# Optimization experiments

Hardware: AMD Instinct MI355X
Metric: run time of the kernel (lower is better)

Reference implementation:

```python
import jax, jax.numpy as jnp
import numpy as np

B, C, H, W = 64, 1280, 16, 16
S = H * W  # 256 spatial positions


def setup_inputs() -> dict:
    key = jax.random.key(0)
    kx, kk, kq, kv, kr, ka = jax.random.split(key, 6)
    x = jax.random.normal(kx, (B, C, H, W), dtype=jnp.float32)
    scale = 0.02
    Wk = jax.random.normal(kk, (C, C), dtype=jnp.float32) * scale
    Wq = jax.random.normal(kq, (C, C), dtype=jnp.float32) * scale
    Wv = jax.random.normal(kv, (C, C), dtype=jnp.float32) * scale
    Wr = jax.random.normal(kr, (C, C), dtype=jnp.float32) * scale
    # nn.Parameter(torch.zeros(1)) in the original; init nonzero so the
    # attention branch actually contributes.
    alpha = jax.random.normal(ka, (1,), dtype=jnp.float32) * 0.1
    return {"x": x, "Wk": Wk, "Wq": Wq, "Wv": Wv, "Wr": Wr, "alpha": alpha}


def reference(x, Wk, Wq, Wv, Wr, alpha):
    b, c = x.shape[0], x.shape[1]
    s = x.shape[2] * x.shape[3]
    xf = x.reshape(b, c, s)  # [B, C, S]
    # 1x1 convs == per-position channel matmuls
    K = jnp.einsum("oc,bcs->bos", Wk, xf)  # [B, C, S]
    Q = jnp.einsum("oc,bcs->bos", Wq, xf)
    V = jnp.einsum("oc,bcs->bos", Wv, xf)
    # scores[b,i,j] = sum_c K[b,c,i] * Q[b,c,j]
    scores = jnp.einsum("bci,bcj->bij", K, Q) / (c ** 0.5)  # [B, S, S]
    # torch.nn.Softmax2d on a 3D tensor applies softmax over dim=-3,
    # i.e. across the BATCH axis here (faithful to the original code).
    A = jax.nn.softmax(scores, axis=0)
    # attended[b,c,i] = sum_j A[b,i,j] * V[b,c,j]
    att = jnp.einsum("bij,bcj->bci", A, V)  # [B, C, S]
    refined = jnp.einsum("oc,bcs->bos", Wr, att).reshape(x.shape)
    out = alpha * refined + x  # use_alpha=True, skip connection
    return out
```

## Files before the change

kernel.cpp:

```cpp
#include <hip/hip_runtime.h>
#include <hip/hip_bf16.h>
#include <cstdint>
#include <cmath>

#define B_ 64
#define C_ 1280
#define S_ 256

typedef __attribute__((ext_vector_type(8))) short short8;
typedef __attribute__((ext_vector_type(4))) float f32x4;

typedef const __attribute__((address_space(1))) char gch;
typedef __attribute__((address_space(3))) char lch;

__device__ __forceinline__ void gload_lds16(const void* g, void* l) {
    __builtin_amdgcn_global_load_lds((gch*)g, (lch*)l, 16, 0, 0);
}

__device__ __forceinline__ unsigned short f2bu(float f) {
    __hip_bfloat16 h = __float2bfloat16(f);
    return *reinterpret_cast<unsigned short*>(&h);
}

__global__ void prep_weights(const float* __restrict__ Wk, const float* __restrict__ Wq,
                             const float* __restrict__ Wv, const float* __restrict__ Wr,
                             __hip_bfloat16* __restrict__ WqT, __hip_bfloat16* __restrict__ WkT,
                             __hip_bfloat16* __restrict__ WvT, __hip_bfloat16* __restrict__ Wrb) {
    __shared__ float tile[32][33];
    int z = blockIdx.z;
    const float* src = (z == 0) ? Wq : (z == 1) ? Wk : (z == 2) ? Wv : Wr;
    __hip_bfloat16* dst = (z == 0) ? WqT : (z == 1) ? WkT : (z == 2) ? WvT : Wrb;
    int r0 = blockIdx.x * 32, c0 = blockIdx.y * 32;
    int tx = threadIdx.x, ty = threadIdx.y;
    if (z == 3) {
#pragma unroll
        for (int dy = 0; dy < 32; dy += 8) {
            int idx = (r0 + ty + dy) * C_ + c0 + tx;
            dst[idx] = __float2bfloat16(src[idx]);
        }
        return;
    }
#pragma unroll
    for (int dy = 0; dy < 32; dy += 8)
        tile[ty + dy][tx] = src[(long)(r0 + ty + dy) * C_ + c0 + tx];
    __syncthreads();
#pragma unroll
    for (int dy = 0; dy < 32; dy += 8)
        dst[(long)(c0 + ty + dy) * C_ + r0 + tx] = __float2bfloat16(tile[tx][ty + dy]);
}

__global__ void transpose_cvt(const float* __restrict__ x, __hip_bfloat16* __restrict__ xT) {
    __shared__ float tile[32][33];
    int b = blockIdx.z;
    int s0 = blockIdx.x * 32, c0 = blockIdx.y * 32;
    int tx = threadIdx.x, ty = threadIdx.y;
    const float* xb = x + (long)b * C_ * S_;
#pragma unroll
    for (int dy = 0; dy < 32; dy += 8)
        tile[ty + dy][tx] = xb[(long)(c0 + ty + dy) * S_ + s0 + tx];
    __syncthreads();
    __hip_bfloat16* xTb = xT + (long)b * S_ * C_;
#pragma unroll
    for (int dy = 0; dy < 32; dy += 8)
        xTb[(long)(s0 + ty + dy) * C_ + c0 + tx] = __float2bfloat16(tile[tx][ty + dy]);
}

__global__ void softmax_b(const float* __restrict__ scores, __hip_bfloat16* __restrict__ Abf) {
    int tid = blockIdx.x * blockDim.x + threadIdx.x;
    float r[64];
    float mx = -1e30f;
#pragma unroll
    for (int b = 0; b < 64; ++b) {
        r[b] = scores[(long)b * 65536 + tid];
        mx = fmaxf(mx, r[b]);
    }
    float sum = 0.f;
#pragma unroll
    for (int b = 0; b < 64; ++b) {
        r[b] = __expf(r[b] - mx);
        sum += r[b];
    }
    float inv = 1.0f / sum;
#pragma unroll
    for (int b = 0; b < 64; ++b)
        Abf[(long)b * 65536 + tid] = __float2bfloat16(r[b] * inv);
}


#define PH_TOP()                                                \
    do {                                                        \
        __builtin_amdgcn_sched_barrier(0);                      \
        __builtin_amdgcn_s_barrier();                           \
        asm volatile("s_waitcnt lgkmcnt(0)" ::: "memory");      \
        __builtin_amdgcn_sched_barrier(0);                      \
        __builtin_amdgcn_s_setprio(1);                          \
    } while (0)

#define PH_BOT()                                                \
    do {                                                        \
        __builtin_amdgcn_s_setprio(0);                          \
        __builtin_amdgcn_sched_barrier(0);                      \
        __builtin_amdgcn_s_barrier();                           \
    } while (0)

#define PH_BOT_WAIT(LAST_)                                          \
    do {                                                            \
        __builtin_amdgcn_s_setprio(0);                              \
        __builtin_amdgcn_sched_barrier(0);                          \
        if (LAST_) asm volatile("s_waitcnt vmcnt(0)" ::: "memory"); \
        else       asm volatile("s_waitcnt vmcnt(2)" ::: "memory"); \
        __builtin_amdgcn_s_barrier();                               \
    } while (0)

#define MFMA_Q(MO, NO, BFV)                                                                        \
    _Pragma("unroll") for (int m = 0; m < 4; ++m) {                                                \
        _Pragma("unroll") for (int n = 0; n < 2; ++n) {                                            \
            acc[m + MO][n + NO] = __builtin_amdgcn_mfma_f32_16x16x32_bf16(                         \
                af[m][0], BFV[n][0], acc[m + MO][n + NO], 0, 0, 0);                                \
            acc[m + MO][n + NO] = __builtin_amdgcn_mfma_f32_16x16x32_bf16(                         \
                af[m][1], BFV[n][1], acc[m + MO][n + NO], 0, 0, 0);                                \
        }                                                                                          \
    }

#define LOAD_A(SLOT, RO)                                  \
    _Pragma("unroll") for (int m = 0; m < 4; ++m) {       \
        af[m][0] = RD(SLOT, (RO) + m * 16 + l15, 0);      \
        af[m][1] = RD(SLOT, (RO) + m * 16 + l15, 1);      \
    }

#define LOAD_B(SLOT, BFV, NO)                                    \
    _Pragma("unroll") for (int n = 0; n < 2; ++n) {              \
        BFV[n][0] = RD(SLOT, rB0 + ((NO) + n) * 16 + l15, 0);    \
        BFV[n][1] = RD(SLOT, rB0 + ((NO) + n) * 16 + l15, 1);    \
    }

__global__ __launch_bounds__(512, 2) void gemm8p(
    const __hip_bfloat16* __restrict__ A, const __hip_bfloat16* __restrict__ Bm,
    __hip_bfloat16* __restrict__ Cc, int lda, int ldb, int ldc,
    int Kd, int tilesN, int nwg, int vTile,
    __hip_bfloat16* __restrict__ Vb) {
    __shared__ char lds[131072];

    int bid = blockIdx.x;
    int cpx = nwg >> 3;
    int swz = (bid & 7) * cpx + (bid >> 3);
    int tm = swz / tilesN, tn = swz - tm * tilesN;

    int t = threadIdx.x;
    int lane = t & 63, w = t >> 6;
    int wm = w >> 2, wn = w & 3;
    int l15 = lane & 15, lhi = lane >> 4;
    int rB0 = (wn & 1) * 64;
    const int sA0 = wm, sB0 = 2 + (wn >> 1);
    const int sA1 = 4 + wm, sB1 = 6 + (wn >> 1);

    const __hip_bfloat16* aT = A + (long)tm * 256 * lda;
    const __hip_bfloat16* bT = Bm + (long)tn * 256 * ldb;

    int srow = t >> 3;
    int sc = ((t & 7) ^ (srow & 7)) * 8;
    const __hip_bfloat16* stA = aT + (long)srow * lda + sc;
    const __hip_bfloat16* stB = bT + (long)srow * ldb + sc;

    auto STAGE = [&](int kt, int j) {
        const __hip_bfloat16* p;
        long ldg;
        if (j < 2) { p = stA + (long)j * 128 * lda + kt * 64; ldg = lda; }
        else       { p = stB + (long)(j - 2) * 128 * ldb + kt * 64; ldg = ldb; }
        char* slot = lds + (((kt & 1) * 4 + j) << 14);
        gload_lds16(p, slot + t * 16);
        gload_lds16(p + 64 * ldg, slot + t * 16 + 8192);
    };

    auto RD = [&](int slotIdx, int row, int kk) -> short8 {
        const char* p = lds + (slotIdx << 14) + row * 128 +
                        ((((kk << 2) + lhi) ^ (row & 7)) << 4);
        return *reinterpret_cast<const short8*>(p);
    };

    f32x4 acc[8][4];
#pragma unroll
    for (int i = 0; i < 8; ++i)
#pragma unroll
        for (int j = 0; j < 4; ++j) acc[i][j] = (f32x4){0.f, 0.f, 0.f, 0.f};

    short8 af[4][2], b0v[2][2], b1v[2][2];

    STAGE(0, 0); STAGE(0, 1); STAGE(0, 2); STAGE(0, 3); STAGE(1, 0);
    asm volatile("s_waitcnt vmcnt(2)" ::: "memory");
    __builtin_amdgcn_s_barrier();
    __builtin_amdgcn_sched_barrier(0);

    const int NTH = Kd >> 7;
    for (int i = 0; i < NTH; ++i) {
        const bool last = (i == NTH - 1);
        const int kt0 = 2 * i, kt1 = 2 * i + 1;

        LOAD_A(sA0, 0)
        LOAD_B(sB0, b0v, 0)
        STAGE(kt1, 1);
        PH_TOP();
        MFMA_Q(0, 0, b0v)
        PH_BOT();

        LOAD_B(sB0, b1v, 2)
        STAGE(kt1, 2);
        PH_TOP();
        MFMA_Q(0, 2, b1v)
        PH_BOT();

        LOAD_A(sA0, 64)
        STAGE(kt1, 3);
        PH_TOP();
        MFMA_Q(4, 2, b1v)
        PH_BOT();

        if (!last) STAGE(kt0 + 2, 0);
        PH_TOP();
        MFMA_Q(4, 0, b0v)
        PH_BOT_WAIT(last);

        LOAD_A(sA1, 0)
        LOAD_B(sB1, b0v, 0)
        if (!last) STAGE(kt0 + 2, 1);
        PH_TOP();
        MFMA_Q(0, 0, b0v)
        PH_BOT();

        LOAD_B(sB1, b1v, 2)
        if (!last) STAGE(kt0 + 2, 2);
        PH_TOP();
        MFMA_Q(0, 2, b1v)
        PH_BOT();

        LOAD_A(sA1, 64)
        if (!last) STAGE(kt0 + 2, 3);
        PH_TOP();
        MFMA_Q(4, 2, b1v)
        PH_BOT();

        if (!last) STAGE(kt0 + 3, 0);
        PH_TOP();
        MFMA_Q(4, 0, b0v)
        __builtin_amdgcn_s_setprio(0);
        __builtin_amdgcn_sched_barrier(0);
        if (!last) asm volatile("s_waitcnt vmcnt(2)" ::: "memory");
        __builtin_amdgcn_s_barrier();
    }

    if (tn < vTile) {
        long crow0 = (long)tm * 256 + wm * 128;
        int cc0 = tn * 256 + wn * 64;
#pragma unroll
        for (int m = 0; m < 8; ++m) {
            long gm = crow0 + m * 16 + lhi * 4;
#pragma unroll
            for (int n = 0; n < 4; ++n) {
                int gn = cc0 + n * 16 + l15;
#pragma unroll
                for (int r = 0; r < 4; ++r)
                    Cc[(gm + r) * ldc + gn] = __float2bfloat16(acc[m][n][r]);
            }
        }
    } else {
        unsigned short* Vus = (unsigned short*)Vb;
        int cb0 = (tn - vTile) * 256 + wn * 64;
#pragma unroll
        for (int m = 0; m < 8; ++m) {
            int s0 = wm * 128 + m * 16 + lhi * 4;
#pragma unroll
            for (int n = 0; n < 4; ++n) {
                int c = cb0 + n * 16 + l15;
                ushort4 pk;
                pk.x = f2bu(acc[m][n][0]);
                pk.y = f2bu(acc[m][n][1]);
                pk.z = f2bu(acc[m][n][2]);
                pk.w = f2bu(acc[m][n][3]);
                *reinterpret_cast<ushort4*>(&Vus[((long)(tm * 1280 + c) << 8) + s0]) = pk;
            }
        }
    }
}

template <int MODE>
__global__ __launch_bounds__(256) void gemm_tn(
    const __hip_bfloat16* __restrict__ A, long aBatch, int lda,
    const __hip_bfloat16* __restrict__ Bm, long bBatch, int ldb,
    void* __restrict__ Cp, long cBatch, int ldc,
    int Kd, int tilesM, int tilesN, float scale) {
    __shared__ __hip_bfloat16 lA[128 * 32];
    __shared__ __hip_bfloat16 lB[128 * 32];

    int tiles = tilesM * tilesN;
    int blk = blockIdx.x;
    int b = blk / tiles;
    int rem = blk - b * tiles;
    int tm = rem / tilesN;
    int tn = rem - tm * tilesN;

    int t = threadIdx.x;
    int lane = t & 63;
    int w = t >> 6;
    int wm = w >> 1, wn = w & 1;
    int lane15 = lane & 15, lhi = lane >> 4;

    const __hip_bfloat16* Ab = A + (long)b * aBatch + (long)tm * 128 * lda;
    const __hip_bfloat16* Bb = Bm + (long)b * bBatch + (long)tn * 128 * ldb;

    f32x4 acc[4][4];
#pragma unroll
    for (int i = 0; i < 4; ++i)
#pragma unroll
        for (int j = 0; j < 4; ++j) acc[i][j] = (f32x4){0.f, 0.f, 0.f, 0.f};

    int e0 = t * 8;
    int r0 = e0 >> 5;
    int c0e = e0 & 31;

    for (int k0 = 0; k0 < Kd; k0 += 32) {
        gload_lds16(Ab + (long)r0 * lda + k0 + c0e, lA + e0);
        gload_lds16(Ab + (long)(r0 + 64) * lda + k0 + c0e, lA + 2048 + e0);
        gload_lds16(Bb + (long)r0 * ldb + k0 + c0e, lB + e0);
        gload_lds16(Bb + (long)(r0 + 64) * ldb + k0 + c0e, lB + 2048 + e0);
        __syncthreads();

        short8 af[4], bf[4];
#pragma unroll
        for (int i = 0; i < 4; ++i)
            af[i] = *reinterpret_cast<const short8*>(lA + (wm * 64 + i * 16 + lane15) * 32 + lhi * 8);
#pragma unroll
        for (int j = 0; j < 4; ++j)
            bf[j] = *reinterpret_cast<const short8*>(lB + (wn * 64 + j * 16 + lane15) * 32 + lhi * 8);
#pragma unroll
        for (int i = 0; i < 4; ++i)
#pragma unroll
            for (int j = 0; j < 4; ++j)
                acc[i][j] = __builtin_amdgcn_mfma_f32_16x16x32_bf16(af[i], bf[j], acc[i][j], 0, 0, 0);
        __syncthreads();
    }

    long cOff = (long)b * cBatch;
    float* Cb = (float*)Cp + cOff;
#pragma unroll
    for (int i = 0; i < 4; ++i) {
        int gm = tm * 128 + wm * 64 + i * 16 + lhi * 4;
#pragma unroll
        for (int j = 0; j < 4; ++j) {
            int gn = tn * 128 + wn * 64 + j * 16 + lane15;
#pragma unroll
            for (int r = 0; r < 4; ++r)
                Cb[(long)(gm + r) * ldc + gn] = acc[i][j][r] * scale;
        }
    }
}

__global__ __launch_bounds__(256) void gemm_weights(
    const __hip_bfloat16* __restrict__ WqT, const __hip_bfloat16* __restrict__ WkT,
    const __hip_bfloat16* __restrict__ Wrb, const __hip_bfloat16* __restrict__ WvT,
    __hip_bfloat16* __restrict__ Bcat, float scale) {
    __shared__ __hip_bfloat16 lA[128 * 32];
    __shared__ __hip_bfloat16 lB[128 * 32];

    int blk = blockIdx.x;
    const __hip_bfloat16 *A, *Bm;
    __hip_bfloat16* Cb;
    float sc;
    int rem;
    if (blk < 100) { A = WqT; Bm = WkT; Cb = Bcat; sc = scale; rem = blk; }
    else { A = Wrb; Bm = WvT; Cb = Bcat + 1280 * 1280; sc = 1.f; rem = blk - 100; }
    int tm = rem / 10, tn = rem - tm * 10;

    int t = threadIdx.x;
    int lane = t & 63;
    int w = t >> 6;
    int wm = w >> 1, wn = w & 1;
    int lane15 = lane & 15, lhi = lane >> 4;

    const __hip_bfloat16* Ab = A + (long)tm * 128 * C_;
    const __hip_bfloat16* Bb = Bm + (long)tn * 128 * C_;

    f32x4 acc[4][4];
#pragma unroll
    for (int i = 0; i < 4; ++i)
#pragma unroll
        for (int j = 0; j < 4; ++j) acc[i][j] = (f32x4){0.f, 0.f, 0.f, 0.f};

    int e0 = t * 8;
    int r0 = e0 >> 5;
    int c0e = e0 & 31;

    for (int k0 = 0; k0 < C_; k0 += 32) {
        gload_lds16(Ab + (long)r0 * C_ + k0 + c0e, lA + e0);
        gload_lds16(Ab + (long)(r0 + 64) * C_ + k0 + c0e, lA + 2048 + e0);
        gload_lds16(Bb + (long)r0 * C_ + k0 + c0e, lB + e0);
        gload_lds16(Bb + (long)(r0 + 64) * C_ + k0 + c0e, lB + 2048 + e0);
        __syncthreads();

        short8 af[4], bf[4];
#pragma unroll
        for (int i = 0; i < 4; ++i)
            af[i] = *reinterpret_cast<const short8*>(lA + (wm * 64 + i * 16 + lane15) * 32 + lhi * 8);
#pragma unroll
        for (int j = 0; j < 4; ++j)
            bf[j] = *reinterpret_cast<const short8*>(lB + (wn * 64 + j * 16 + lane15) * 32 + lhi * 8);
#pragma unroll
        for (int i = 0; i < 4; ++i)
#pragma unroll
            for (int j = 0; j < 4; ++j)
                acc[i][j] = __builtin_amdgcn_mfma_f32_16x16x32_bf16(af[i], bf[j], acc[i][j], 0, 0, 0);
        __syncthreads();
    }

#pragma unroll
    for (int i = 0; i < 4; ++i) {
        int gm = tm * 128 + wm * 64 + i * 16 + lhi * 4;
#pragma unroll
        for (int j = 0; j < 4; ++j) {
            int gn = tn * 128 + wn * 64 + j * 16 + lane15;
#pragma unroll
            for (int r = 0; r < 4; ++r)
                Cb[(long)(gm + r) * C_ + gn] = __float2bfloat16(acc[i][j][r] * sc);
        }
    }
}

__global__ __launch_bounds__(256) void final_att(
    const __hip_bfloat16* __restrict__ Abf, const __hip_bfloat16* __restrict__ P,
    const float* __restrict__ x, const float* __restrict__ alphaPtr,
    float* __restrict__ out) {
    __shared__ __hip_bfloat16 lA[128 * 32];
    __shared__ __hip_bfloat16 lB[128 * 32];

    int blk = blockIdx.x;
    int b = blk / 20;
    int rem = blk - b * 20;
    int tm = rem / 10, tn = rem - tm * 10;

    int t = threadIdx.x;
    int lane = t & 63;
    int w = t >> 6;
    int wm = w >> 1, wn = w & 1;
    int lane15 = lane & 15, lhi = lane >> 4;

    const __hip_bfloat16* Ab = Abf + (long)b * (S_ * S_) + (long)tm * 128 * S_;
    const __hip_bfloat16* Bb = P + (long)b * (C_ * S_) + (long)tn * 128 * S_;

    f32x4 acc[4][4];
#pragma unroll
    for (int i = 0; i < 4; ++i)
#pragma unroll
        for (int j = 0; j < 4; ++j) acc[i][j] = (f32x4){0.f, 0.f, 0.f, 0.f};

    int e0 = t * 8;
    int r0 = e0 >> 5;
    int c0e = e0 & 31;

#pragma unroll
    for (int k0 = 0; k0 < S_; k0 += 32) {
        gload_lds16(Ab + (long)r0 * S_ + k0 + c0e, lA + e0);
        gload_lds16(Ab + (long)(r0 + 64) * S_ + k0 + c0e, lA + 2048 + e0);
        gload_lds16(Bb + (long)r0 * S_ + k0 + c0e, lB + e0);
        gload_lds16(Bb + (long)(r0 + 64) * S_ + k0 + c0e, lB + 2048 + e0);
        __syncthreads();

        short8 af[4], bf[4];
#pragma unroll
        for (int i = 0; i < 4; ++i)
            af[i] = *reinterpret_cast<const short8*>(lA + (wm * 64 + i * 16 + lane15) * 32 + lhi * 8);
#pragma unroll
        for (int j = 0; j < 4; ++j)
            bf[j] = *reinterpret_cast<const short8*>(lB + (wn * 64 + j * 16 + lane15) * 32 + lhi * 8);
#pragma unroll
        for (int i = 0; i < 4; ++i)
#pragma unroll
            for (int j = 0; j < 4; ++j)
                acc[i][j] = __builtin_amdgcn_mfma_f32_16x16x32_bf16(af[i], bf[j], acc[i][j], 0, 0, 0);
        __syncthreads();
    }

    float alpha = alphaPtr[0];
    long bOff = (long)b * (C_ * S_);
#pragma unroll
    for (int i = 0; i < 4; ++i) {
        int s0 = tm * 128 + wm * 64 + i * 16 + lhi * 4;
#pragma unroll
        for (int j = 0; j < 4; ++j) {
            int c = tn * 128 + wn * 64 + j * 16 + lane15;
            long base = bOff + (long)c * S_ + s0;
            f32x4 xv = *reinterpret_cast<const f32x4*>(x + base);
            f32x4 o;
#pragma unroll
            for (int r = 0; r < 4; ++r) o[r] = alpha * acc[i][j][r] + xv[r];
            *reinterpret_cast<f32x4*>(out + base) = o;
        }
    }
}

extern "C" void kernel_launch(void* const* d_in, const int* in_sizes, int n_in,
                              void* d_out, int out_size, void* d_ws, size_t ws_size,
                              hipStream_t stream) {
    const float* x = (const float*)d_in[0];
    const float* Wk = (const float*)d_in[1];
    const float* Wq = (const float*)d_in[2];
    const float* Wv = (const float*)d_in[3];
    const float* Wr = (const float*)d_in[4];
    const float* alphaPtr = (const float*)d_in[5];

    char* ws = (char*)d_ws;
    size_t off = 0;
    auto alloc = [&](size_t bytes) {
        char* p = ws + off;
        off += (bytes + 255) & ~(size_t)255;
        return p;
    };
    const size_t BSC = (size_t)B_ * S_ * C_;
    const size_t CC = (size_t)C_ * C_;

    __hip_bfloat16* xT = (__hip_bfloat16*)alloc(BSC * 2);
    __hip_bfloat16* WqT = (__hip_bfloat16*)alloc(CC * 2);
    __hip_bfloat16* WkT = (__hip_bfloat16*)alloc(CC * 2);
    __hip_bfloat16* WvT = (__hip_bfloat16*)alloc(CC * 2);
    __hip_bfloat16* Wrb = (__hip_bfloat16*)alloc(CC * 2);
    __hip_bfloat16* Bcat = (__hip_bfloat16*)alloc(2 * CC * 2);
    __hip_bfloat16* G = (__hip_bfloat16*)alloc(BSC * 2);
    __hip_bfloat16* P = (__hip_bfloat16*)alloc(BSC * 2);
    float* scores = (float*)alloc((size_t)B_ * S_ * S_ * 4);
    __hip_bfloat16* Abf = (__hip_bfloat16*)alloc((size_t)B_ * S_ * S_ * 2);

    const float scale = 1.0f / sqrtf((float)C_);

    prep_weights<<<dim3(40, 40, 4), dim3(32, 8), 0, stream>>>(Wk, Wq, Wv, Wr,
                                                              WqT, WkT, WvT, Wrb);
    gemm_weights<<<200, 256, 0, stream>>>(WqT, WkT, Wrb, WvT, Bcat, scale);

    transpose_cvt<<<dim3(S_ / 32, C_ / 32, B_), dim3(32, 8), 0, stream>>>(x, xT);

    gemm8p<<<640, 512, 0, stream>>>(xT, Bcat, G, C_, C_, C_, C_, 10, 640, 5, P);

    gemm_tn<1><<<B_ * 4, 256, 0, stream>>>(G, (long)S_ * C_, C_,
                                           xT, (long)S_ * C_, C_,
                                           scores, (long)S_ * S_, S_,
                                           C_, 2, 2, 1.0f);
    softmax_b<<<256, 256, 0, stream>>>(scores, Abf);

    final_att<<<1280, 256, 0, stream>>>(Abf, P, x, alphaPtr, (float*)d_out);
}
```

Measured before the change: 431.6 us.

## Double-buffer and swizzle LDS in GEMMs, merge prep kernels, widen final tile

```diff
diff --git a/kernel.cpp b/kernel.cpp
--- a/kernel.cpp
+++ b/kernel.cpp
@@ -22,47 +22,50 @@
     return *reinterpret_cast<unsigned short*>(&h);
 }
 
-__global__ void prep_weights(const float* __restrict__ Wk, const float* __restrict__ Wq,
-                             const float* __restrict__ Wv, const float* __restrict__ Wr,
-                             __hip_bfloat16* __restrict__ WqT, __hip_bfloat16* __restrict__ WkT,
-                             __hip_bfloat16* __restrict__ WvT, __hip_bfloat16* __restrict__ Wrb) {
+__global__ void prep_x(const float* __restrict__ x, __hip_bfloat16* __restrict__ xT,
+                       const float* __restrict__ Wk, const float* __restrict__ Wq,
+                       const float* __restrict__ Wv, const float* __restrict__ Wr,
+                       __hip_bfloat16* __restrict__ WqT, __hip_bfloat16* __restrict__ WkT,
+                       __hip_bfloat16* __restrict__ WvT, __hip_bfloat16* __restrict__ Wrb) {
     __shared__ float tile[32][33];
-    int z = blockIdx.z;
-    const float* src = (z == 0) ? Wq : (z == 1) ? Wk : (z == 2) ? Wv : Wr;
-    __hip_bfloat16* dst = (z == 0) ? WqT : (z == 1) ? WkT : (z == 2) ? WvT : Wrb;
-    int r0 = blockIdx.x * 32, c0 = blockIdx.y * 32;
+    int id = blockIdx.x;
     int tx = threadIdx.x, ty = threadIdx.y;
-    if (z == 3) {
-#pragma unroll
-        for (int dy = 0; dy < 32; dy += 8) {
-            int idx = (r0 + ty + dy) * C_ + c0 + tx;
-            dst[idx] = __float2bfloat16(src[idx]);
+    if (id < 20480) {
+        int b = id / 320;
+        int rem = id - b * 320;
+        int s0 = (rem & 7) * 32, c0 = (rem >> 3) * 32;
+        const float* xb = x + (long)b * C_ * S_;
+#pragma unroll
+        for (int dy = 0; dy < 32; dy += 8)
+            tile[ty + dy][tx] = xb[(long)(c0 + ty + dy) * S_ + s0 + tx];
+        __syncthreads();
+        __hip_bfloat16* xTb = xT + (long)b * S_ * C_;
+#pragma unroll
+        for (int dy = 0; dy < 32; dy += 8)
+            xTb[(long)(s0 + ty + dy) * C_ + c0 + tx] = __float2bfloat16(tile[tx][ty + dy]);
+    } else {
+        int wid = id - 20480;
+        int z = wid / 1600;
+        int rem = wid - z * 1600;
+        int r0 = (rem / 40) * 32, c0 = (rem - (rem / 40) * 40) * 32;
+        const float* src = (z == 0) ? Wq : (z == 1) ? Wk : (z == 2) ? Wv : Wr;
+        __hip_bfloat16* dst = (z == 0) ? WqT : (z == 1) ? WkT : (z == 2) ? WvT : Wrb;
+        if (z == 3) {
+#pragma unroll
+            for (int dy = 0; dy < 32; dy += 8) {
+                int idx = (r0 + ty + dy) * C_ + c0 + tx;
+                dst[idx] = __float2bfloat16(src[idx]);
+            }
+            return;
         }
-        return;
-    }
-#pragma unroll
-    for (int dy = 0; dy < 32; dy += 8)
-        tile[ty + dy][tx] = src[(long)(r0 + ty + dy) * C_ + c0 + tx];
-    __syncthreads();
-#pragma unroll
-    for (int dy = 0; dy < 32; dy += 8)
-        dst[(long)(c0 + ty + dy) * C_ + r0 + tx] = __float2bfloat16(tile[tx][ty + dy]);
-}
-
-__global__ void transpose_cvt(const float* __restrict__ x, __hip_bfloat16* __restrict__ xT) {
-    __shared__ float tile[32][33];
-    int b = blockIdx.z;
-    int s0 = blockIdx.x * 32, c0 = blockIdx.y * 32;
-    int tx = threadIdx.x, ty = threadIdx.y;
-    const float* xb = x + (long)b * C_ * S_;
-#pragma unroll
-    for (int dy = 0; dy < 32; dy += 8)
-        tile[ty + dy][tx] = xb[(long)(c0 + ty + dy) * S_ + s0 + tx];
-    __syncthreads();
-    __hip_bfloat16* xTb = xT + (long)b * S_ * C_;
-#pragma unroll
-    for (int dy = 0; dy < 32; dy += 8)
-        xTb[(long)(s0 + ty + dy) * C_ + c0 + tx] = __float2bfloat16(tile[tx][ty + dy]);
+#pragma unroll
+        for (int dy = 0; dy < 32; dy += 8)
+            tile[ty + dy][tx] = src[(long)(r0 + ty + dy) * C_ + c0 + tx];
+        __syncthreads();
+#pragma unroll
+        for (int dy = 0; dy < 32; dy += 8)
+            dst[(long)(c0 + ty + dy) * C_ + r0 + tx] = __float2bfloat16(tile[tx][ty + dy]);
+    }
 }
 
 __global__ void softmax_b(const float* __restrict__ scores, __hip_bfloat16* __restrict__ Abf) {
@@ -282,30 +285,31 @@
     }
 }
 
-template <int MODE>
-__global__ __launch_bounds__(256) void gemm_tn(
-    const __hip_bfloat16* __restrict__ A, long aBatch, int lda,
-    const __hip_bfloat16* __restrict__ Bm, long bBatch, int ldb,
-    void* __restrict__ Cp, long cBatch, int ldc,
-    int Kd, int tilesM, int tilesN, float scale) {
-    __shared__ __hip_bfloat16 lA[128 * 32];
-    __shared__ __hip_bfloat16 lB[128 * 32];
-
-    int tiles = tilesM * tilesN;
+__global__ __launch_bounds__(256) void gemm_scores(
+    const __hip_bfloat16* __restrict__ G, const __hip_bfloat16* __restrict__ xT,
+    float* __restrict__ scores, float scale) {
+    __shared__ __hip_bfloat16 lA[2][4096];
+    __shared__ __hip_bfloat16 lB[2][4096];
+
     int blk = blockIdx.x;
-    int b = blk / tiles;
-    int rem = blk - b * tiles;
-    int tm = rem / tilesN;
-    int tn = rem - tm * tilesN;
-
-    int t = threadIdx.x;
-    int lane = t & 63;
-    int w = t >> 6;
+    int b = blk >> 2, tm = (blk >> 1) & 1, tn = blk & 1;
+    int t = threadIdx.x, lane = t & 63, w = t >> 6;
     int wm = w >> 1, wn = w & 1;
-    int lane15 = lane & 15, lhi = lane >> 4;
-
-    const __hip_bfloat16* Ab = A + (long)b * aBatch + (long)tm * 128 * lda;
-    const __hip_bfloat16* Bb = Bm + (long)b * bBatch + (long)tn * 128 * ldb;
+    int l15 = lane & 15, lhi = lane >> 4;
+    int kx = (lhi ^ (l15 & 3)) << 4;
+
+    const __hip_bfloat16* Ab = G + (long)b * (S_ * C_) + (long)tm * 128 * C_;
+    const __hip_bfloat16* Bb = xT + (long)b * (S_ * C_) + (long)tn * 128 * C_;
+
+    int arow = t >> 2;
+    int acol = ((t & 3) ^ (arow & 3)) * 8;
+
+    auto STAGE = [&](int k0, int buf) {
+        gload_lds16(Ab + (long)arow * C_ + k0 + acol, (char*)lA[buf] + t * 16);
+        gload_lds16(Ab + (long)(arow + 64) * C_ + k0 + acol, (char*)lA[buf] + t * 16 + 4096);
+        gload_lds16(Bb + (long)arow * C_ + k0 + acol, (char*)lB[buf] + t * 16);
+        gload_lds16(Bb + (long)(arow + 64) * C_ + k0 + acol, (char*)lB[buf] + t * 16 + 4096);
+    };
 
     f32x4 acc[4][4];
 #pragma unroll
@@ -313,24 +317,22 @@
 #pragma unroll
         for (int j = 0; j < 4; ++j) acc[i][j] = (f32x4){0.f, 0.f, 0.f, 0.f};
 
-    int e0 = t * 8;
-    int r0 = e0 >> 5;
-    int c0e = e0 & 31;
-
-    for (int k0 = 0; k0 < Kd; k0 += 32) {
-        gload_lds16(Ab + (long)r0 * lda + k0 + c0e, lA + e0);
-        gload_lds16(Ab + (long)(r0 + 64) * lda + k0 + c0e, lA + 2048 + e0);
-        gload_lds16(Bb + (long)r0 * ldb + k0 + c0e, lB + e0);
-        gload_lds16(Bb + (long)(r0 + 64) * ldb + k0 + c0e, lB + 2048 + e0);
-        __syncthreads();
-
+    STAGE(0, 0);
+    __syncthreads();
+
+#pragma unroll 2
+    for (int k = 0; k < 40; ++k) {
+        int cur = k & 1;
+        if (k < 39) STAGE((k + 1) * 32, cur ^ 1);
         short8 af[4], bf[4];
 #pragma unroll
         for (int i = 0; i < 4; ++i)
-            af[i] = *reinterpret_cast<const short8*>(lA + (wm * 64 + i * 16 + lane15) * 32 + lhi * 8);
+            af[i] = *reinterpret_cast<const short8*>(
+                (const char*)lA[cur] + (wm * 64 + i * 16 + l15) * 64 + kx);
 #pragma unroll
         for (int j = 0; j < 4; ++j)
-            bf[j] = *reinterpret_cast<const short8*>(lB + (wn * 64 + j * 16 + lane15) * 32 + lhi * 8);
+            bf[j] = *reinterpret_cast<const short8*>(
+                (const char*)lB[cur] + (wn * 64 + j * 16 + l15) * 64 + kx);
 #pragma unroll
         for (int i = 0; i < 4; ++i)
 #pragma unroll
@@ -339,17 +341,16 @@
         __syncthreads();
     }
 
-    long cOff = (long)b * cBatch;
-    float* Cb = (float*)Cp + cOff;
+    float* Cb = scores + (long)b * 65536;
 #pragma unroll
     for (int i = 0; i < 4; ++i) {
         int gm = tm * 128 + wm * 64 + i * 16 + lhi * 4;
 #pragma unroll
         for (int j = 0; j < 4; ++j) {
-            int gn = tn * 128 + wn * 64 + j * 16 + lane15;
+            int gn = tn * 128 + wn * 64 + j * 16 + l15;
 #pragma unroll
             for (int r = 0; r < 4; ++r)
-                Cb[(long)(gm + r) * ldc + gn] = acc[i][j][r] * scale;
+                Cb[(long)(gm + r) * 256 + gn] = acc[i][j][r] * scale;
         }
     }
 }
@@ -358,8 +359,8 @@
     const __hip_bfloat16* __restrict__ WqT, const __hip_bfloat16* __restrict__ WkT,
     const __hip_bfloat16* __restrict__ Wrb, const __hip_bfloat16* __restrict__ WvT,
     __hip_bfloat16* __restrict__ Bcat, float scale) {
-    __shared__ __hip_bfloat16 lA[128 * 32];
-    __shared__ __hip_bfloat16 lB[128 * 32];
+    __shared__ __hip_bfloat16 lA[2][4096];
+    __shared__ __hip_bfloat16 lB[2][4096];
 
     int blk = blockIdx.x;
     const __hip_bfloat16 *A, *Bm;
@@ -370,39 +371,46 @@
     else { A = Wrb; Bm = WvT; Cb = Bcat + 1280 * 1280; sc = 1.f; rem = blk - 100; }
     int tm = rem / 10, tn = rem - tm * 10;
 
-    int t = threadIdx.x;
-    int lane = t & 63;
-    int w = t >> 6;
+    int t = threadIdx.x, lane = t & 63, w = t >> 6;
     int wm = w >> 1, wn = w & 1;
-    int lane15 = lane & 15, lhi = lane >> 4;
+    int l15 = lane & 15, lhi = lane >> 4;
+    int kx = (lhi ^ (l15 & 3)) << 4;
 
     const __hip_bfloat16* Ab = A + (long)tm * 128 * C_;
     const __hip_bfloat16* Bb = Bm + (long)tn * 128 * C_;
 
+    int arow = t >> 2;
+    int acol = ((t & 3) ^ (arow & 3)) * 8;
+
+    auto STAGE = [&](int k0, int buf) {
+        gload_lds16(Ab + (long)arow * C_ + k0 + acol, (char*)lA[buf] + t * 16);
+        gload_lds16(Ab + (long)(arow + 64) * C_ + k0 + acol, (char*)lA[buf] + t * 16 + 4096);
+        gload_lds16(Bb + (long)arow * C_ + k0 + acol, (char*)lB[buf] + t * 16);
+        gload_lds16(Bb + (long)(arow + 64) * C_ + k0 + acol, (char*)lB[buf] + t * 16 + 4096);
+    };
+
     f32x4 acc[4][4];
 #pragma unroll
     for (int i = 0; i < 4; ++i)
 #pragma unroll
         for (int j = 0; j < 4; ++j) acc[i][j] = (f32x4){0.f, 0.f, 0.f, 0.f};
 
-    int e0 = t * 8;
-    int r0 = e0 >> 5;
-    int c0e = e0 & 31;
-
-    for (int k0 = 0; k0 < C_; k0 += 32) {
-        gload_lds16(Ab + (long)r0 * C_ + k0 + c0e, lA + e0);
-        gload_lds16(Ab + (long)(r0 + 64) * C_ + k0 + c0e, lA + 2048 + e0);
-        gload_lds16(Bb + (long)r0 * C_ + k0 + c0e, lB + e0);
-        gload_lds16(Bb + (long)(r0 + 64) * C_ + k0 + c0e, lB + 2048 + e0);
-        __syncthreads();
-
+    STAGE(0, 0);
+    __syncthreads();
+
+#pragma unroll 2
+    for (int k = 0; k < 40; ++k) {
+        int cur = k & 1;
+        if (k < 39) STAGE((k + 1) * 32, cur ^ 1);
         short8 af[4], bf[4];
 #pragma unroll
         for (int i = 0; i < 4; ++i)
-            af[i] = *reinterpret_cast<const short8*>(lA + (wm * 64 + i * 16 + lane15) * 32 + lhi * 8);
+            af[i] = *reinterpret_cast<const short8*>(
+                (const char*)lA[cur] + (wm * 64 + i * 16 + l15) * 64 + kx);
 #pragma unroll
         for (int j = 0; j < 4; ++j)
-            bf[j] = *reinterpret_cast<const short8*>(lB + (wn * 64 + j * 16 + lane15) * 32 + lhi * 8);
+            bf[j] = *reinterpret_cast<const short8*>(
+                (const char*)lB[cur] + (wn * 64 + j * 16 + l15) * 64 + kx);
 #pragma unroll
         for (int i = 0; i < 4; ++i)
 #pragma unroll
@@ -416,7 +424,7 @@
         int gm = tm * 128 + wm * 64 + i * 16 + lhi * 4;
 #pragma unroll
         for (int j = 0; j < 4; ++j) {
-            int gn = tn * 128 + wn * 64 + j * 16 + lane15;
+            int gn = tn * 128 + wn * 64 + j * 16 + l15;
 #pragma unroll
             for (int r = 0; r < 4; ++r)
                 Cb[(long)(gm + r) * C_ + gn] = __float2bfloat16(acc[i][j][r] * sc);
@@ -424,57 +432,65 @@
     }
 }
 
-__global__ __launch_bounds__(256) void final_att(
+__global__ __launch_bounds__(256, 2) void final_att2(
     const __hip_bfloat16* __restrict__ Abf, const __hip_bfloat16* __restrict__ P,
     const float* __restrict__ x, const float* __restrict__ alphaPtr,
     float* __restrict__ out) {
-    __shared__ __hip_bfloat16 lA[128 * 32];
-    __shared__ __hip_bfloat16 lB[128 * 32];
+    __shared__ __hip_bfloat16 lA[2][4096];
+    __shared__ __hip_bfloat16 lB[2][8192];
 
     int blk = blockIdx.x;
-    int b = blk / 20;
-    int rem = blk - b * 20;
-    int tm = rem / 10, tn = rem - tm * 10;
-
-    int t = threadIdx.x;
-    int lane = t & 63;
-    int w = t >> 6;
+    int b = blk / 10;
+    int rem = blk - b * 10;
+    int tm = rem / 5, tnp = rem - tm * 5;
+
+    int t = threadIdx.x, lane = t & 63, w = t >> 6;
     int wm = w >> 1, wn = w & 1;
-    int lane15 = lane & 15, lhi = lane >> 4;
-
-    const __hip_bfloat16* Ab = Abf + (long)b * (S_ * S_) + (long)tm * 128 * S_;
-    const __hip_bfloat16* Bb = P + (long)b * (C_ * S_) + (long)tn * 128 * S_;
-
-    f32x4 acc[4][4];
+    int l15 = lane & 15, lhi = lane >> 4;
+    int kx = (lhi ^ (l15 & 3)) << 4;
+
+    const __hip_bfloat16* Ab = Abf + (long)b * 65536 + (long)tm * 128 * 256;
+    const __hip_bfloat16* Bb = P + (long)b * (C_ * S_) + (long)tnp * 256 * 256;
+
+    int arow = t >> 2;
+    int acol = ((t & 3) ^ (arow & 3)) * 8;
+
+    auto STAGE = [&](int k0, int buf) {
+        gload_lds16(Ab + (long)arow * 256 + k0 + acol, (char*)lA[buf] + t * 16);
+        gload_lds16(Ab + (long)(arow + 64) * 256 + k0 + acol, (char*)lA[buf] + t * 16 + 4096);
+#pragma unroll
+        for (int j = 0; j < 4; ++j)
+            gload_lds16(Bb + (long)(arow + j * 64) * 256 + k0 + acol,
+                        (char*)lB[buf] + t * 16 + j * 4096);
+    };
+
+    f32x4 acc[4][8];
 #pragma unroll
     for (int i = 0; i < 4; ++i)
 #pragma unroll
-        for (int j = 0; j < 4; ++j) acc[i][j] = (f32x4){0.f, 0.f, 0.f, 0.f};
-
-    int e0 = t * 8;
-    int r0 = e0 >> 5;
-    int c0e = e0 & 31;
-
-#pragma unroll
-    for (int k0 = 0; k0 < S_; k0 += 32) {
-        gload_lds16(Ab + (long)r0 * S_ + k0 + c0e, lA + e0);
-        gload_lds16(Ab + (long)(r0 + 64) * S_ + k0 + c0e, lA + 2048 + e0);
-        gload_lds16(Bb + (long)r0 * S_ + k0 + c0e, lB + e0);
-        gload_lds16(Bb + (long)(r0 + 64) * S_ + k0 + c0e, lB + 2048 + e0);
-        __syncthreads();
-
-        short8 af[4], bf[4];
+        for (int n = 0; n < 8; ++n) acc[i][n] = (f32x4){0.f, 0.f, 0.f, 0.f};
+
+    STAGE(0, 0);
+    __syncthreads();
+
+#pragma unroll
+    for (int k = 0; k < 8; ++k) {
+        int cur = k & 1;
+        if (k < 7) STAGE((k + 1) * 32, cur ^ 1);
+        short8 af[4], bf[8];
 #pragma unroll
         for (int i = 0; i < 4; ++i)
-            af[i] = *reinterpret_cast<const short8*>(lA + (wm * 64 + i * 16 + lane15) * 32 + lhi * 8);
-#pragma unroll
-        for (int j = 0; j < 4; ++j)
-            bf[j] = *reinterpret_cast<const short8*>(lB + (wn * 64 + j * 16 + lane15) * 32 + lhi * 8);
+            af[i] = *reinterpret_cast<const short8*>(
+                (const char*)lA[cur] + (wm * 64 + i * 16 + l15) * 64 + kx);
+#pragma unroll
+        for (int n = 0; n < 8; ++n)
+            bf[n] = *reinterpret_cast<const short8*>(
+                (const char*)lB[cur] + (wn * 128 + n * 16 + l15) * 64 + kx);
 #pragma unroll
         for (int i = 0; i < 4; ++i)
 #pragma unroll
-            for (int j = 0; j < 4; ++j)
-                acc[i][j] = __builtin_amdgcn_mfma_f32_16x16x32_bf16(af[i], bf[j], acc[i][j], 0, 0, 0);
+            for (int n = 0; n < 8; ++n)
+                acc[i][n] = __builtin_amdgcn_mfma_f32_16x16x32_bf16(af[i], bf[n], acc[i][n], 0, 0, 0);
         __syncthreads();
     }
 
@@ -484,13 +500,13 @@
     for (int i = 0; i < 4; ++i) {
         int s0 = tm * 128 + wm * 64 + i * 16 + lhi * 4;
 #pragma unroll
-        for (int j = 0; j < 4; ++j) {
-            int c = tn * 128 + wn * 64 + j * 16 + lane15;
-            long base = bOff + (long)c * S_ + s0;
+        for (int n = 0; n < 8; ++n) {
+            int c = tnp * 256 + wn * 128 + n * 16 + l15;
+            long base = bOff + (long)c * 256 + s0;
             f32x4 xv = *reinterpret_cast<const f32x4*>(x + base);
             f32x4 o;
 #pragma unroll
-            for (int r = 0; r < 4; ++r) o[r] = alpha * acc[i][j][r] + xv[r];
+            for (int r = 0; r < 4; ++r) o[r] = alpha * acc[i][n][r] + xv[r];
             *reinterpret_cast<f32x4*>(out + base) = o;
         }
     }
@@ -529,19 +545,15 @@
 
     const float scale = 1.0f / sqrtf((float)C_);
 
-    prep_weights<<<dim3(40, 40, 4), dim3(32, 8), 0, stream>>>(Wk, Wq, Wv, Wr,
-                                                              WqT, WkT, WvT, Wrb);
+    prep_x<<<26880, dim3(32, 8), 0, stream>>>(x, xT, Wk, Wq, Wv, Wr, WqT, WkT, WvT, Wrb);
+
     gemm_weights<<<200, 256, 0, stream>>>(WqT, WkT, Wrb, WvT, Bcat, scale);
 
-    transpose_cvt<<<dim3(S_ / 32, C_ / 32, B_), dim3(32, 8), 0, stream>>>(x, xT);
-
     gemm8p<<<640, 512, 0, stream>>>(xT, Bcat, G, C_, C_, C_, C_, 10, 640, 5, P);
 
-    gemm_tn<1><<<B_ * 4, 256, 0, stream>>>(G, (long)S_ * C_, C_,
-                                           xT, (long)S_ * C_, C_,
-                                           scores, (long)S_ * S_, S_,
-                                           C_, 2, 2, 1.0f);
+    gemm_scores<<<256, 256, 0, stream>>>(G, xT, scores, 1.0f);
+
     softmax_b<<<256, 256, 0, stream>>>(scores, Abf);
 
-    final_att<<<1280, 256, 0, stream>>>(Abf, P, x, alphaPtr, (float*)d_out);
-}
+    final_att2<<<640, 256, 0, stream>>>(Abf, P, x, alphaPtr, (float*)d_out);
+}
```

New measurement: 423.4 us. About the same (-1.9%).
